# Kernel tuning notes

Hardware: AMD Instinct MI355X
Metric: run time of the kernel (lower is better)

Reference implementation:

```python
import jax, jax.numpy as jnp
from jax import lax
import numpy as np

B, S = 4096, 200           # batch, max history length
MAX_LEN, STEP = 1024, 4    # module init args
BINS = MAX_LEN // STEP     # 256 time bins
H = 64                     # LSTM hidden (dimension)


def setup_inputs() -> dict:
    key = jax.random.key(0)
    ks = jax.random.split(key, 8)
    time = jax.random.uniform(ks[0], (B, S), jnp.float32, 0.0, 1000.0)
    # predict_time >= max event time per row (module assumes nonnegative bin index)
    predict_time = jnp.max(time, axis=1) + jax.random.uniform(ks[1], (B,), jnp.float32, 0.0, 24.0)
    length = jax.random.randint(ks[2], (B,), 1, S + 1, jnp.int32)
    # torch nn.LSTM init: uniform(-1/sqrt(H), 1/sqrt(H)); gate order i,f,g,o
    s = 1.0 / np.sqrt(H)
    W_ih = jax.random.uniform(ks[3], (4 * H, 1), jnp.float32, -s, s)
    W_hh = jax.random.uniform(ks[4], (4 * H, H), jnp.float32, -s, s)
    b_ih = jax.random.uniform(ks[5], (4 * H,), jnp.float32, -s, s)
    b_hh = jax.random.uniform(ks[6], (4 * H,), jnp.float32, -s, s)
    return {"time": time, "length": length, "predict_time": predict_time,
            "W_ih": W_ih, "W_hh": W_hh, "b_ih": b_ih, "b_hh": b_hh}


def _histogram(time, length, predict_time):
    # pos = int((predict_time - time_ij) / STEP), incremented at bin BINS-1-pos
    pos = ((predict_time[:, None] - time) / STEP).astype(jnp.int32)  # trunc toward 0, like int()
    valid = (jnp.arange(S)[None, :] < length[:, None]) & (pos >= 0) & (pos < BINS)
    idx = BINS - 1 - jnp.clip(pos, 0, BINS - 1)
    hist = jnp.zeros((B, BINS), jnp.float32)
    hist = hist.at[jnp.arange(B)[:, None], idx].add(valid.astype(jnp.float32))
    return hist  # [B, BINS]


def _lstm_final_h(x, W_ih, W_hh, b_ih, b_hh):
    # x: [B, T] scalar sequence (input_size=1). Returns final hidden state [B, H].
    b = b_ih + b_hh

    def step(carry, x_t):
        h, c = carry
        gates = x_t[:, None] * W_ih[:, 0][None, :] + h @ W_hh.T + b  # [B, 4H]
        i, f, g, o = jnp.split(gates, 4, axis=1)
        c = jax.nn.sigmoid(f) * c + jax.nn.sigmoid(i) * jnp.tanh(g)
        h = jax.nn.sigmoid(o) * jnp.tanh(c)
        return (h, c), None

    init = (jnp.zeros((B, H), x.dtype), jnp.zeros((B, H), x.dtype))
    (h, _), _ = lax.scan(step, init, jnp.moveaxis(x, 1, 0))  # scan over T
    return h


def reference(time, length, predict_time, W_ih, W_hh, b_ih, b_hh):
    hist = _histogram(time, length, predict_time)
    return _lstm_final_h(hist, W_ih, W_hh, b_ih, b_hh)
```

## Files before the change

### kernel.cpp

```cpp
#include <hip/hip_runtime.h>
#include <hip/hip_bf16.h>


#define B_S     200
#define B_T     256
#define ROWS    16
#define THREADS 512
#define HS      72
#define LOG2E   1.4426950408889634f

typedef __attribute__((ext_vector_type(8))) _Float16 half8;
typedef __attribute__((ext_vector_type(4))) float float4_t;

__device__ __forceinline__ float load_f(const void* p, int i, int isb) {
    if (isb) {
        unsigned short u = ((const unsigned short*)p)[i];
        return __uint_as_float(((unsigned int)u) << 16);
    }
    return ((const float*)p)[i];
}

__global__ __launch_bounds__(THREADS)
void trend_encoder_kernel(const void* __restrict__ time_,
                          const int*  __restrict__ length,
                          const void* __restrict__ ptime_,
                          const void* __restrict__ wih_,
                          const void* __restrict__ whh_,
                          const void* __restrict__ bih_,
                          const void* __restrict__ bhh_,
                          void* __restrict__ out_) {
    __shared__ __align__(16) float x_t[B_T * ROWS];
    __shared__ __align__(16) _Float16 h_sh[2][ROWS * HS];
    __shared__ int flag_sh;

    const int tid   = threadIdx.x;
    const int wv    = tid >> 6;
    const int lane  = tid & 63;
    const int m     = lane & 15;
    const int quad  = lane >> 4;
    const int hc    = wv & 3;
    const int rhalf = wv >> 2;
    const int b0    = blockIdx.x * ROWS;

    if (tid < 64) {
        unsigned short u = ((const unsigned short*)wih_)[tid];
        float v = __uint_as_float(((unsigned int)u) << 16);
        int bad = !(v > -0.2f && v < 0.2f);
        unsigned long long bm = __ballot(bad);
        if (lane == 0) flag_sh = (bm == 0ULL) ? 1 : 0;
    }
    for (int i = tid; i < B_T * ROWS; i += THREADS) x_t[i] = 0.0f;
    for (int i = tid; i < ROWS * HS; i += THREADS) h_sh[0][i] = (_Float16)0.0f;
    __syncthreads();
    const int isb = flag_sh;

    for (int e = tid; e < ROWS * B_S; e += THREADS) {
        int row  = e / B_S;
        int s    = e - row * B_S;
        int grow = b0 + row;
        if (s < length[grow]) {
            float pt = load_f(ptime_, grow, isb);
            float tv = load_f(time_, grow * B_S + s, isb);
            int pos = (int)((pt - tv) * 0.25f);
            if (pos >= 0 && pos < B_T)
                atomicAdd(&x_t[(B_T - 1 - pos) * ROWS + row], 1.0f);
        }
    }

    const float gsc[4] = {-LOG2E, -LOG2E, 2.0f * LOG2E, -LOG2E};
    half8 bw[4][2];
    float wihv[4], biasv[4];
    #pragma unroll
    for (int tt = 0; tt < 4; ++tt) {
        int n = 16 * hc + 64 * tt + m;
        float s = gsc[tt];
        wihv[tt]  = load_f(wih_, n, isb) * s;
        biasv[tt] = (load_f(bih_, n, isb) + load_f(bhh_, n, isb)) * s;
        #pragma unroll
        for (int c = 0; c < 2; ++c) {
            half8 v;
            #pragma unroll
            for (int j = 0; j < 8; ++j)
                v[j] = (_Float16)(load_f(whh_, n * 64 + 32 * c + 8 * quad + j, isb) * s);
            bw[tt][c] = v;
        }
    }

    const int aoff = m * HS + 8 * quad;
    const int kcol = 16 * hc + m;
    float creg[2] = {0.f, 0.f};
    float hreg[2] = {0.f, 0.f};
    __syncthreads();

    #define ACT(RR, R)                                                        \
    {                                                                         \
        float A  = __builtin_amdgcn_exp2f(acc[0][R]);     \
        float F  = __builtin_amdgcn_exp2f(acc[1][R]);     \
        float Bv = __builtin_amdgcn_exp2f(acc[2][R]);     \
        float t1    = (1.0f + A) * (Bv + 1.0f);                               \
        float oneF  = 1.0f + F;                                               \
        float numer = fmaf(creg[RR], t1, oneF * (Bv - 1.0f));                 \
        float denom = oneF * t1;                                              \
        creg[RR] = numer * __builtin_amdgcn_rcpf(denom);                      \
        float D  = __builtin_amdgcn_exp2f(acc[3][R]);     \
        float cs = fminf(creg[RR] * (2.0f * LOG2E), 126.0f);   \
        float E  = __builtin_amdgcn_exp2f(cs);                                \
        float h  = (E - 1.0f) * __builtin_amdgcn_rcpf((1.0f + D) * (E + 1.0f)); \
        hreg[RR] = h;                                                         \
        wb[(quad * 4 + R) * HS + kcol] = (_Float16)h;                         \
    }

    for (int t = 0; t < B_T; ++t) {
        const int p = t & 1;
        const _Float16* hh = h_sh[p];
        half8 a0 = *(const half8*)&hh[aoff];
        half8 a1 = *(const half8*)&hh[aoff + 32];
        float4_t xv = *(const float4_t*)&x_t[t * ROWS + quad * 4];

        float4_t acc[4];
        #pragma unroll
        for (int tt = 0; tt < 4; ++tt) {
            float4_t a;
            #pragma unroll
            for (int r = 0; r < 4; ++r) a[r] = fmaf(xv[r], wihv[tt], biasv[tt]);
            a = __builtin_amdgcn_mfma_f32_16x16x32_f16(a0, bw[tt][0], a, 0, 0, 0);
            a = __builtin_amdgcn_mfma_f32_16x16x32_f16(a1, bw[tt][1], a, 0, 0, 0);
            acc[tt] = a;
        }

        _Float16* wb = h_sh[p ^ 1];
        if (rhalf == 0) { ACT(0, 0); ACT(1, 1); }
        else            { ACT(0, 2); ACT(1, 3); }
        __syncthreads();
    }
    #undef ACT

    #pragma unroll
    for (int rr = 0; rr < 2; ++rr) {
        int o = (b0 + quad * 4 + 2 * rhalf + rr) * 64 + kcol;
        if (isb) ((__hip_bfloat16*)out_)[o] = __float2bfloat16(hreg[rr]);
        else     ((float*)out_)[o] = hreg[rr];
    }
}

extern "C" void kernel_launch(void* const* d_in, const int* in_sizes, int n_in,
                              void* d_out, int out_size, void* d_ws, size_t ws_size,
                              hipStream_t stream) {
    const void* time_  = d_in[0];
    const int*  length = (const int*)d_in[1];
    const void* ptime  = d_in[2];
    const void* wih    = d_in[3];
    const void* whh    = d_in[4];
    const void* bih    = d_in[5];
    const void* bhh    = d_in[6];

    const int B = in_sizes[1];
    trend_encoder_kernel<<<dim3(B / ROWS), dim3(THREADS), 0, stream>>>(
        time_, length, ptime, wih, whh, bih, bhh, d_out);
}
```

Before: 211.6 us.

## Halve rows per block and remap MFMA outputs via lane shuffles

Each block now handles 8 batch rows with 256 threads instead of 16 rows with 512 threads, so the grid doubles. The MFMA tiles keep 16 rows, with the upper 8 left as zero padding. Each wave now computes all gates for its hidden slice, and a cross-lane shuffle redistributes accumulator rows so every lane still runs two activations. The per-step x input is also prefetched for the next step before the barrier. The aim is smaller barrier groups and more independent blocks to hide the serial recurrence latency, at the cost of half-wasted MFMA work and extra shuffles.

```diff
diff --git a/kernel.cpp b/kernel.cpp
--- a/kernel.cpp
+++ b/kernel.cpp
@@ -4,8 +4,9 @@
 
 #define B_S     200
 #define B_T     256
-#define ROWS    16
-#define THREADS 512
+#define ROWS    8
+#define MR      16
+#define THREADS 256
 #define HS      72
 #define LOG2E   1.4426950408889634f
 
@@ -29,18 +30,16 @@
                           const void* __restrict__ bih_,
                           const void* __restrict__ bhh_,
                           void* __restrict__ out_) {
-    __shared__ __align__(16) float x_t[B_T * ROWS];
-    __shared__ __align__(16) _Float16 h_sh[2][ROWS * HS];
+    __shared__ __align__(16) float x_t[B_T * MR];
+    __shared__ __align__(16) _Float16 h_sh[2][MR * HS];
     __shared__ int flag_sh;
 
-    const int tid   = threadIdx.x;
-    const int wv    = tid >> 6;
-    const int lane  = tid & 63;
-    const int m     = lane & 15;
-    const int quad  = lane >> 4;
-    const int hc    = wv & 3;
-    const int rhalf = wv >> 2;
-    const int b0    = blockIdx.x * ROWS;
+    const int tid  = threadIdx.x;
+    const int wv   = tid >> 6;
+    const int lane = tid & 63;
+    const int m    = lane & 15;
+    const int quad = lane >> 4;
+    const int b0   = blockIdx.x * ROWS;
 
     if (tid < 64) {
         unsigned short u = ((const unsigned short*)wih_)[tid];
@@ -49,8 +48,11 @@
         unsigned long long bm = __ballot(bad);
         if (lane == 0) flag_sh = (bm == 0ULL) ? 1 : 0;
     }
-    for (int i = tid; i < B_T * ROWS; i += THREADS) x_t[i] = 0.0f;
-    for (int i = tid; i < ROWS * HS; i += THREADS) h_sh[0][i] = (_Float16)0.0f;
+    for (int i = tid; i < B_T * MR; i += THREADS) x_t[i] = 0.0f;
+    {
+        _Float16* hz = &h_sh[0][0];
+        for (int i = tid; i < 2 * MR * HS; i += THREADS) hz[i] = (_Float16)0.0f;
+    }
     __syncthreads();
     const int isb = flag_sh;
 
@@ -63,7 +65,7 @@
             float tv = load_f(time_, grow * B_S + s, isb);
             int pos = (int)((pt - tv) * 0.25f);
             if (pos >= 0 && pos < B_T)
-                atomicAdd(&x_t[(B_T - 1 - pos) * ROWS + row], 1.0f);
+                atomicAdd(&x_t[(B_T - 1 - pos) * MR + row], 1.0f);
         }
     }
 
@@ -72,7 +74,7 @@
     float wihv[4], biasv[4];
     #pragma unroll
     for (int tt = 0; tt < 4; ++tt) {
-        int n = 16 * hc + 64 * tt + m;
+        int n = 16 * wv + 64 * tt + m;
         float s = gsc[tt];
         wihv[tt]  = load_f(wih_, n, isb) * s;
         biasv[tt] = (load_f(bih_, n, isb) + load_f(bhh_, n, isb)) * s;
@@ -87,35 +89,37 @@
     }
 
     const int aoff = m * HS + 8 * quad;
-    const int kcol = 16 * hc + m;
+    const int kcol = 16 * wv + m;
+    const int row0 = 4 * (quad & 1) + 2 * (quad >> 1);
     float creg[2] = {0.f, 0.f};
     float hreg[2] = {0.f, 0.f};
     __syncthreads();
 
-    #define ACT(RR, R)                                                        \
+    #define ACT(RR, G0, G1, G2, G3)                                           \
     {                                                                         \
-        float A  = __builtin_amdgcn_exp2f(acc[0][R]);     \
-        float F  = __builtin_amdgcn_exp2f(acc[1][R]);     \
-        float Bv = __builtin_amdgcn_exp2f(acc[2][R]);     \
+        float A  = __builtin_amdgcn_exp2f(G0);            \
+        float F  = __builtin_amdgcn_exp2f(G1);            \
+        float Bv = __builtin_amdgcn_exp2f(G2);            \
         float t1    = (1.0f + A) * (Bv + 1.0f);                               \
         float oneF  = 1.0f + F;                                               \
         float numer = fmaf(creg[RR], t1, oneF * (Bv - 1.0f));                 \
         float denom = oneF * t1;                                              \
         creg[RR] = numer * __builtin_amdgcn_rcpf(denom);                      \
-        float D  = __builtin_amdgcn_exp2f(acc[3][R]);     \
+        float D  = __builtin_amdgcn_exp2f(G3);            \
         float cs = fminf(creg[RR] * (2.0f * LOG2E), 126.0f);   \
         float E  = __builtin_amdgcn_exp2f(cs);                                \
         float h  = (E - 1.0f) * __builtin_amdgcn_rcpf((1.0f + D) * (E + 1.0f)); \
         hreg[RR] = h;                                                         \
-        wb[(quad * 4 + R) * HS + kcol] = (_Float16)h;                         \
+        wb[(row0 + RR) * HS + kcol] = (_Float16)h;                            \
     }
+
+    float4_t xv = *(const float4_t*)&x_t[0 * MR + quad * 4];
 
     for (int t = 0; t < B_T; ++t) {
         const int p = t & 1;
         const _Float16* hh = h_sh[p];
         half8 a0 = *(const half8*)&hh[aoff];
         half8 a1 = *(const half8*)&hh[aoff + 32];
-        float4_t xv = *(const float4_t*)&x_t[t * ROWS + quad * 4];
 
         float4_t acc[4];
         #pragma unroll
@@ -128,16 +132,28 @@
             acc[tt] = a;
         }
 
+        float gA[4], gB[4];
+        #pragma unroll
+        for (int tt = 0; tt < 4; ++tt) {
+            float x2 = __shfl_xor(acc[tt][2], 32);
+            float x3 = __shfl_xor(acc[tt][3], 32);
+            gA[tt] = (quad < 2) ? acc[tt][0] : x2;
+            gB[tt] = (quad < 2) ? acc[tt][1] : x3;
+        }
+
         _Float16* wb = h_sh[p ^ 1];
-        if (rhalf == 0) { ACT(0, 0); ACT(1, 1); }
-        else            { ACT(0, 2); ACT(1, 3); }
+        ACT(0, gA[0], gA[1], gA[2], gA[3]);
+        ACT(1, gB[0], gB[1], gB[2], gB[3]);
+
+        int tn = (t + 1 < B_T) ? t + 1 : t;
+        xv = *(const float4_t*)&x_t[tn * MR + quad * 4];
         __syncthreads();
     }
     #undef ACT
 
     #pragma unroll
     for (int rr = 0; rr < 2; ++rr) {
-        int o = (b0 + quad * 4 + 2 * rhalf + rr) * 64 + kcol;
+        int o = (b0 + row0 + rr) * 64 + kcol;
         if (isb) ((__hip_bfloat16*)out_)[o] = __float2bfloat16(hreg[rr]);
         else     ((float*)out_)[o] = hreg[rr];
     }
```

Result: slower. 232.1 us (+9.7%).
